# Optimization experiments

Hardware: AMD Instinct MI355X
Metric: run time of the kernel (lower is better)

The kernel has to match this reference:

```python
import jax, jax.numpy as jnp
import numpy as np

SPARSITY = 0.8  # fraction of weights zeroed (random unstructured mask)

def setup_inputs() -> dict:
    key = jax.random.key(0)
    k1, k2, k3, k4 = jax.random.split(key, 4)
    B, S, D_IN, D_OUT = 4, 2048, 4096, 4096
    x = jax.random.normal(k1, (B, S, D_IN), dtype=jnp.float32)
    weight = jax.random.normal(k2, (D_OUT, D_IN), dtype=jnp.float32) * 0.02
    bias = jax.random.normal(k3, (D_OUT,), dtype=jnp.float32) * 0.02
    # fixed binary mask: keep with prob (1 - sparsity)
    mask = (jax.random.uniform(k4, (D_OUT, D_IN)) >= SPARSITY).astype(jnp.float32)
    return {"x": x, "weight": weight, "bias": bias, "mask": mask}

def reference(x, weight, bias, mask):
    # w = weight * mask; y = x @ w.T + b   (F.linear semantics)
    w = weight * mask                      # [O, I]
    y = jnp.einsum('bsi,oi->bso', x, w)    # [B, S, O]
    return y + bias
```

## Files before the change

kernel.cpp:

```cpp
#include <hip/hip_runtime.h>
#include <hip/hip_bf16.h>
#include <stdint.h>

#define M_DIM 8192
#define N_DIM 4096
#define K_DIM 4096
#define BM 128
#define BN 128
#define BK 32

typedef __attribute__((ext_vector_type(8))) __bf16 bf16x8;
typedef __attribute__((ext_vector_type(4))) float floatx4;

__device__ inline unsigned f2b(float f) {
    union { float f; unsigned u; } v; v.f = f;
    return (v.u + 0x7FFFu + ((v.u >> 16) & 1u)) >> 16;
}
__device__ inline unsigned pk2(float lo, float hi) {
    return (f2b(lo) & 0xFFFFu) | (f2b(hi) << 16);
}

__device__ inline void async_load16(const void* g, void* l) {
    __builtin_amdgcn_global_load_lds(
        (const __attribute__((address_space(1))) unsigned int*)(unsigned long long)g,
        (__attribute__((address_space(3))) unsigned int*)(unsigned int)(unsigned long long)l,
        16, 0, 0);
}

__global__ __launch_bounds__(256)
void cvt_x_kernel(const float4* __restrict__ in, uint4* __restrict__ out, int n8) {
    int i = blockIdx.x * blockDim.x + threadIdx.x;
    if (i >= n8) return;
    float4 a = in[2 * i], b = in[2 * i + 1];
    uint4 o;
    o.x = pk2(a.x, a.y); o.y = pk2(a.z, a.w);
    o.z = pk2(b.x, b.y); o.w = pk2(b.z, b.w);
    out[i] = o;
}

__global__ __launch_bounds__(256)
void cvt_w_kernel(const float4* __restrict__ w, const float4* __restrict__ m,
                  uint4* __restrict__ out, int n8) {
    int i = blockIdx.x * blockDim.x + threadIdx.x;
    if (i >= n8) return;
    float4 w0 = w[2 * i], w1 = w[2 * i + 1];
    float4 m0 = m[2 * i], m1 = m[2 * i + 1];
    uint4 o;
    o.x = pk2(w0.x * m0.x, w0.y * m0.y);
    o.y = pk2(w0.z * m0.z, w0.w * m0.w);
    o.z = pk2(w1.x * m1.x, w1.y * m1.y);
    o.w = pk2(w1.z * m1.z, w1.w * m1.w);
    out[i] = o;
}

__global__ __launch_bounds__(256)
void gemm_bt_bias(const __hip_bfloat16* __restrict__ A,
                  const __hip_bfloat16* __restrict__ B,
                  const float* __restrict__ bias,
                  float* __restrict__ C) {
    __shared__ __hip_bfloat16 As[BM * BK];
    __shared__ __hip_bfloat16 Bs[BN * BK];

    const int t    = threadIdx.x;
    const int lane = t & 63;
    const int wave = t >> 6;
    const int wm   = wave >> 1;
    const int wn   = wave & 1;
    const int m0   = blockIdx.y * BM;
    const int n0   = blockIdx.x * BN;

    const int lm = lane & 15;
    const int lk = (lane >> 4) << 3;

    floatx4 acc[4][4] = {};

    const int c0 = t, c1 = t + 256;
    const int ar0 = c0 >> 2, ak0 = (c0 & 3) << 3;
    const int ar1 = c1 >> 2, ak1 = (c1 & 3) << 3;

    const __hip_bfloat16* Ab = A + (size_t)m0 * K_DIM;
    const __hip_bfloat16* Bb = B + (size_t)n0 * K_DIM;

    for (int k0 = 0; k0 < K_DIM; k0 += BK) {
        async_load16(Ab + (size_t)ar0 * K_DIM + k0 + ak0, As + c0 * 8);
        async_load16(Ab + (size_t)ar1 * K_DIM + k0 + ak1, As + c1 * 8);
        async_load16(Bb + (size_t)ar0 * K_DIM + k0 + ak0, Bs + c0 * 8);
        async_load16(Bb + (size_t)ar1 * K_DIM + k0 + ak1, Bs + c1 * 8);
        __syncthreads();

        bf16x8 af[4], bfr[4];
#pragma unroll
        for (int i = 0; i < 4; i++)
            af[i] = *reinterpret_cast<const bf16x8*>(
                &As[(wm * 64 + i * 16 + lm) * BK + lk]);
#pragma unroll
        for (int j = 0; j < 4; j++)
            bfr[j] = *reinterpret_cast<const bf16x8*>(
                &Bs[(wn * 64 + j * 16 + lm) * BK + lk]);
#pragma unroll
        for (int i = 0; i < 4; i++)
#pragma unroll
            for (int j = 0; j < 4; j++)
                acc[i][j] = __builtin_amdgcn_mfma_f32_16x16x32_bf16(
                    af[i], bfr[j], acc[i][j], 0, 0, 0);
        __syncthreads();
    }

    float bv[4];
#pragma unroll
    for (int j = 0; j < 4; j++)
        bv[j] = bias[n0 + wn * 64 + j * 16 + lm];
    const int row_base = m0 + wm * 64 + (lane >> 4) * 4;
    const int col_base = n0 + wn * 64 + lm;
#pragma unroll
    for (int i = 0; i < 4; i++)
#pragma unroll
        for (int j = 0; j < 4; j++) {
            const int col = col_base + j * 16;
#pragma unroll
            for (int r = 0; r < 4; r++)
                C[(size_t)(row_base + i * 16 + r) * N_DIM + col] =
                    acc[i][j][r] + bv[j];
        }
}

__global__ __launch_bounds__(256)
void gemm_fused_f32(const float* __restrict__ A, const float* __restrict__ W,
                    const float* __restrict__ Mk, const float* __restrict__ bias,
                    float* __restrict__ C) {
    __shared__ __hip_bfloat16 As[BM * BK];
    __shared__ __hip_bfloat16 Bs[BN * BK];

    const int t    = threadIdx.x;
    const int lane = t & 63;
    const int wave = t >> 6;
    const int wm   = wave >> 1;
    const int wn   = wave & 1;
    const int m0   = blockIdx.y * BM;
    const int n0   = blockIdx.x * BN;
    const int lm = lane & 15;
    const int lk = (lane >> 4) << 3;

    floatx4 acc[4][4] = {};

    const int r  = t >> 1;
    const int cb = (t & 1) * 16;

    for (int k0 = 0; k0 < K_DIM; k0 += BK) {
        const float* ap = A + (size_t)(m0 + r) * K_DIM + k0 + cb;
        float4 f0 = ((const float4*)ap)[0], f1 = ((const float4*)ap)[1];
        float4 f2 = ((const float4*)ap)[2], f3 = ((const float4*)ap)[3];
        uint4 pa, pb;
        pa.x = pk2(f0.x, f0.y); pa.y = pk2(f0.z, f0.w);
        pa.z = pk2(f1.x, f1.y); pa.w = pk2(f1.z, f1.w);
        pb.x = pk2(f2.x, f2.y); pb.y = pk2(f2.z, f2.w);
        pb.z = pk2(f3.x, f3.y); pb.w = pk2(f3.z, f3.w);
        *(uint4*)&As[r * BK + cb] = pa;
        *(uint4*)&As[r * BK + cb + 8] = pb;

        const float* wp = W + (size_t)(n0 + r) * K_DIM + k0 + cb;
        const float* mp = Mk + (size_t)(n0 + r) * K_DIM + k0 + cb;
        float4 w0 = ((const float4*)wp)[0], w1 = ((const float4*)wp)[1];
        float4 w2 = ((const float4*)wp)[2], w3 = ((const float4*)wp)[3];
        float4 q0 = ((const float4*)mp)[0], q1 = ((const float4*)mp)[1];
        float4 q2 = ((const float4*)mp)[2], q3 = ((const float4*)mp)[3];
        pa.x = pk2(w0.x * q0.x, w0.y * q0.y); pa.y = pk2(w0.z * q0.z, w0.w * q0.w);
        pa.z = pk2(w1.x * q1.x, w1.y * q1.y); pa.w = pk2(w1.z * q1.z, w1.w * q1.w);
        pb.x = pk2(w2.x * q2.x, w2.y * q2.y); pb.y = pk2(w2.z * q2.z, w2.w * q2.w);
        pb.z = pk2(w3.x * q3.x, w3.y * q3.y); pb.w = pk2(w3.z * q3.z, w3.w * q3.w);
        *(uint4*)&Bs[r * BK + cb] = pa;
        *(uint4*)&Bs[r * BK + cb + 8] = pb;
        __syncthreads();

        bf16x8 af[4], bfr[4];
#pragma unroll
        for (int i = 0; i < 4; i++)
            af[i] = *reinterpret_cast<const bf16x8*>(
                &As[(wm * 64 + i * 16 + lm) * BK + lk]);
#pragma unroll
        for (int j = 0; j < 4; j++)
            bfr[j] = *reinterpret_cast<const bf16x8*>(
                &Bs[(wn * 64 + j * 16 + lm) * BK + lk]);
#pragma unroll
        for (int i = 0; i < 4; i++)
#pragma unroll
            for (int j = 0; j < 4; j++)
                acc[i][j] = __builtin_amdgcn_mfma_f32_16x16x32_bf16(
                    af[i], bfr[j], acc[i][j], 0, 0, 0);
        __syncthreads();
    }

    float bv[4];
#pragma unroll
    for (int j = 0; j < 4; j++)
        bv[j] = bias[n0 + wn * 64 + j * 16 + lm];
    const int row_base = m0 + wm * 64 + (lane >> 4) * 4;
    const int col_base = n0 + wn * 64 + lm;
#pragma unroll
    for (int i = 0; i < 4; i++)
#pragma unroll
        for (int j = 0; j < 4; j++) {
            const int col = col_base + j * 16;
#pragma unroll
            for (int r4 = 0; r4 < 4; r4++)
                C[(size_t)(row_base + i * 16 + r4) * N_DIM + col] =
                    acc[i][j][r4] + bv[j];
        }
}

extern "C" void kernel_launch(void* const* d_in, const int* in_sizes, int n_in,
                              void* d_out, int out_size, void* d_ws, size_t ws_size,
                              hipStream_t stream) {
    const float* x    = (const float*)d_in[0];
    const float* w    = (const float*)d_in[1];
    const float* bias = (const float*)d_in[2];
    const float* mask = (const float*)d_in[3];
    float* out = (float*)d_out;

    const size_t xb_bytes = (size_t)M_DIM * K_DIM * 2;
    const size_t wb_bytes = (size_t)N_DIM * K_DIM * 2;
    dim3 grid(N_DIM / BN, M_DIM / BM);
    dim3 block(256);

    if (ws_size >= xb_bytes + wb_bytes) {
        __hip_bfloat16* xb = (__hip_bfloat16*)d_ws;
        __hip_bfloat16* wb = (__hip_bfloat16*)((char*)d_ws + xb_bytes);

        const int nx8 = M_DIM * K_DIM / 8;
        cvt_x_kernel<<<dim3(nx8 / 256), block, 0, stream>>>(
            (const float4*)x, (uint4*)xb, nx8);
        const int nw8 = N_DIM * K_DIM / 8;
        cvt_w_kernel<<<dim3(nw8 / 256), block, 0, stream>>>(
            (const float4*)w, (const float4*)mask, (uint4*)wb, nw8);
        gemm_bt_bias<<<grid, block, 0, stream>>>(xb, wb, bias, out);
    } else {
        gemm_fused_f32<<<grid, block, 0, stream>>>(x, w, mask, bias, out);
    }
}
```

Measured before the change: 624.3 us.

## Pre-pack bf16 operands into swizzled tile panels and merge conversion kernels

```diff
diff --git a/kernel.cpp b/kernel.cpp
--- a/kernel.cpp
+++ b/kernel.cpp
@@ -8,6 +8,8 @@
 #define BM 128
 #define BN 128
 #define BK 32
+#define KP (K_DIM / BK)
+#define PANEL_U4 512
 
 typedef __attribute__((ext_vector_type(8))) __bf16 bf16x8;
 typedef __attribute__((ext_vector_type(4))) float floatx4;
@@ -18,6 +20,12 @@
 }
 __device__ inline unsigned pk2(float lo, float hi) {
     return (f2b(lo) & 0xFFFFu) | (f2b(hi) << 16);
+}
+__device__ inline uint4 pk8(float4 a, float4 b) {
+    uint4 o;
+    o.x = pk2(a.x, a.y); o.y = pk2(a.z, a.w);
+    o.z = pk2(b.x, b.y); o.w = pk2(b.z, b.w);
+    return o;
 }
 
 __device__ inline void async_load16(const void* g, void* l) {
@@ -28,34 +36,42 @@
 }
 
 __global__ __launch_bounds__(256)
-void cvt_x_kernel(const float4* __restrict__ in, uint4* __restrict__ out, int n8) {
-    int i = blockIdx.x * blockDim.x + threadIdx.x;
-    if (i >= n8) return;
-    float4 a = in[2 * i], b = in[2 * i + 1];
-    uint4 o;
-    o.x = pk2(a.x, a.y); o.y = pk2(a.z, a.w);
-    o.z = pk2(b.x, b.y); o.w = pk2(b.z, b.w);
-    out[i] = o;
+void cvt_pack_kernel(const float* __restrict__ x,
+                     const float* __restrict__ w,
+                     const float* __restrict__ mask,
+                     uint4* __restrict__ xb, uint4* __restrict__ wb) {
+    const int NX = M_DIM * K_DIM / 8;
+    int tid = blockIdx.x * 256 + threadIdx.x;
+    if (tid < NX) {
+        const int cx = tid;
+        const int p = cx >> 9, s = cx & 511;
+        const int r4 = s >> 2, perm = s & 3;
+        const int ksub = perm ^ ((r4 >> 1) & 3);
+        const int rt = p >> 7, kp = p & (KP - 1);
+        const size_t src = (size_t)(rt * BM + r4) * K_DIM + kp * BK + ksub * 8;
+        float4 a = *(const float4*)(x + src);
+        float4 b = *(const float4*)(x + src + 4);
+        xb[cx] = pk8(a, b);
+    } else {
+        const int cw = tid - NX;
+        const int p = cw >> 9, s = cw & 511;
+        const int r4 = s >> 2, perm = s & 3;
+        const int ksub = perm ^ ((r4 >> 1) & 3);
+        const int nt = p >> 7, kp = p & (KP - 1);
+        const size_t src = (size_t)(nt * BN + r4) * K_DIM + kp * BK + ksub * 8;
+        float4 a = *(const float4*)(w + src);
+        float4 b = *(const float4*)(w + src + 4);
+        float4 qa = *(const float4*)(mask + src);
+        float4 qb = *(const float4*)(mask + src + 4);
+        a.x *= qa.x; a.y *= qa.y; a.z *= qa.z; a.w *= qa.w;
+        b.x *= qb.x; b.y *= qb.y; b.z *= qb.z; b.w *= qb.w;
+        wb[cw] = pk8(a, b);
+    }
 }
 
 __global__ __launch_bounds__(256)
-void cvt_w_kernel(const float4* __restrict__ w, const float4* __restrict__ m,
-                  uint4* __restrict__ out, int n8) {
-    int i = blockIdx.x * blockDim.x + threadIdx.x;
-    if (i >= n8) return;
-    float4 w0 = w[2 * i], w1 = w[2 * i + 1];
-    float4 m0 = m[2 * i], m1 = m[2 * i + 1];
-    uint4 o;
-    o.x = pk2(w0.x * m0.x, w0.y * m0.y);
-    o.y = pk2(w0.z * m0.z, w0.w * m0.w);
-    o.z = pk2(w1.x * m1.x, w1.y * m1.y);
-    o.w = pk2(w1.z * m1.z, w1.w * m1.w);
-    out[i] = o;
-}
-
-__global__ __launch_bounds__(256)
-void gemm_bt_bias(const __hip_bfloat16* __restrict__ A,
-                  const __hip_bfloat16* __restrict__ B,
+void gemm_bt_bias(const uint4* __restrict__ Apan,
+                  const uint4* __restrict__ Bpan,
                   const float* __restrict__ bias,
                   float* __restrict__ C) {
     __shared__ __hip_bfloat16 As[BM * BK];
@@ -69,34 +85,31 @@
     const int m0   = blockIdx.y * BM;
     const int n0   = blockIdx.x * BN;
 
-    const int lm = lane & 15;
-    const int lk = (lane >> 4) << 3;
+    const int lm   = lane & 15;
+    const int perm = ((lane >> 4) ^ ((lane >> 1) & 3)) & 3;
 
     floatx4 acc[4][4] = {};
 
     const int c0 = t, c1 = t + 256;
-    const int ar0 = c0 >> 2, ak0 = (c0 & 3) << 3;
-    const int ar1 = c1 >> 2, ak1 = (c1 & 3) << 3;
-
-    const __hip_bfloat16* Ab = A + (size_t)m0 * K_DIM;
-    const __hip_bfloat16* Bb = B + (size_t)n0 * K_DIM;
-
-    for (int k0 = 0; k0 < K_DIM; k0 += BK) {
-        async_load16(Ab + (size_t)ar0 * K_DIM + k0 + ak0, As + c0 * 8);
-        async_load16(Ab + (size_t)ar1 * K_DIM + k0 + ak1, As + c1 * 8);
-        async_load16(Bb + (size_t)ar0 * K_DIM + k0 + ak0, Bs + c0 * 8);
-        async_load16(Bb + (size_t)ar1 * K_DIM + k0 + ak1, Bs + c1 * 8);
+    const uint4* ap = Apan + ((size_t)blockIdx.y * KP) * PANEL_U4;
+    const uint4* bp = Bpan + ((size_t)blockIdx.x * KP) * PANEL_U4;
+
+    const __hip_bfloat16* aF = As + (((wm * 64 + lm) * 4 + perm) * 8);
+    const __hip_bfloat16* bF = Bs + (((wn * 64 + lm) * 4 + perm) * 8);
+
+    for (int kp = 0; kp < KP; kp++) {
+        async_load16(ap + c0, As + c0 * 8);
+        async_load16(ap + c1, As + c1 * 8);
+        async_load16(bp + c0, Bs + c0 * 8);
+        async_load16(bp + c1, Bs + c1 * 8);
+        ap += PANEL_U4; bp += PANEL_U4;
         __syncthreads();
 
         bf16x8 af[4], bfr[4];
 #pragma unroll
-        for (int i = 0; i < 4; i++)
-            af[i] = *reinterpret_cast<const bf16x8*>(
-                &As[(wm * 64 + i * 16 + lm) * BK + lk]);
-#pragma unroll
-        for (int j = 0; j < 4; j++)
-            bfr[j] = *reinterpret_cast<const bf16x8*>(
-                &Bs[(wn * 64 + j * 16 + lm) * BK + lk]);
+        for (int i = 0; i < 4; i++) af[i]  = *(const bf16x8*)(aF + i * 512);
+#pragma unroll
+        for (int j = 0; j < 4; j++) bfr[j] = *(const bf16x8*)(bF + j * 512);
 #pragma unroll
         for (int i = 0; i < 4; i++)
 #pragma unroll
@@ -130,57 +143,38 @@
                     float* __restrict__ C) {
     __shared__ __hip_bfloat16 As[BM * BK];
     __shared__ __hip_bfloat16 Bs[BN * BK];
-
-    const int t    = threadIdx.x;
-    const int lane = t & 63;
-    const int wave = t >> 6;
-    const int wm   = wave >> 1;
-    const int wn   = wave & 1;
-    const int m0   = blockIdx.y * BM;
-    const int n0   = blockIdx.x * BN;
-    const int lm = lane & 15;
-    const int lk = (lane >> 4) << 3;
-
+    const int t = threadIdx.x, lane = t & 63, wave = t >> 6;
+    const int wm = wave >> 1, wn = wave & 1;
+    const int m0 = blockIdx.y * BM, n0 = blockIdx.x * BN;
+    const int lm = lane & 15, lk = (lane >> 4) << 3;
     floatx4 acc[4][4] = {};
-
-    const int r  = t >> 1;
-    const int cb = (t & 1) * 16;
-
+    const int r = t >> 1, cb = (t & 1) * 16;
     for (int k0 = 0; k0 < K_DIM; k0 += BK) {
         const float* ap = A + (size_t)(m0 + r) * K_DIM + k0 + cb;
         float4 f0 = ((const float4*)ap)[0], f1 = ((const float4*)ap)[1];
         float4 f2 = ((const float4*)ap)[2], f3 = ((const float4*)ap)[3];
-        uint4 pa, pb;
-        pa.x = pk2(f0.x, f0.y); pa.y = pk2(f0.z, f0.w);
-        pa.z = pk2(f1.x, f1.y); pa.w = pk2(f1.z, f1.w);
-        pb.x = pk2(f2.x, f2.y); pb.y = pk2(f2.z, f2.w);
-        pb.z = pk2(f3.x, f3.y); pb.w = pk2(f3.z, f3.w);
-        *(uint4*)&As[r * BK + cb] = pa;
-        *(uint4*)&As[r * BK + cb + 8] = pb;
-
+        *(uint4*)&As[r * BK + cb] = pk8(f0, f1);
+        *(uint4*)&As[r * BK + cb + 8] = pk8(f2, f3);
         const float* wp = W + (size_t)(n0 + r) * K_DIM + k0 + cb;
         const float* mp = Mk + (size_t)(n0 + r) * K_DIM + k0 + cb;
         float4 w0 = ((const float4*)wp)[0], w1 = ((const float4*)wp)[1];
         float4 w2 = ((const float4*)wp)[2], w3 = ((const float4*)wp)[3];
         float4 q0 = ((const float4*)mp)[0], q1 = ((const float4*)mp)[1];
         float4 q2 = ((const float4*)mp)[2], q3 = ((const float4*)mp)[3];
-        pa.x = pk2(w0.x * q0.x, w0.y * q0.y); pa.y = pk2(w0.z * q0.z, w0.w * q0.w);
-        pa.z = pk2(w1.x * q1.x, w1.y * q1.y); pa.w = pk2(w1.z * q1.z, w1.w * q1.w);
-        pb.x = pk2(w2.x * q2.x, w2.y * q2.y); pb.y = pk2(w2.z * q2.z, w2.w * q2.w);
-        pb.z = pk2(w3.x * q3.x, w3.y * q3.y); pb.w = pk2(w3.z * q3.z, w3.w * q3.w);
-        *(uint4*)&Bs[r * BK + cb] = pa;
-        *(uint4*)&Bs[r * BK + cb + 8] = pb;
-        __syncthreads();
-
+        w0.x*=q0.x; w0.y*=q0.y; w0.z*=q0.z; w0.w*=q0.w;
+        w1.x*=q1.x; w1.y*=q1.y; w1.z*=q1.z; w1.w*=q1.w;
+        w2.x*=q2.x; w2.y*=q2.y; w2.z*=q2.z; w2.w*=q2.w;
+        w3.x*=q3.x; w3.y*=q3.y; w3.z*=q3.z; w3.w*=q3.w;
+        *(uint4*)&Bs[r * BK + cb] = pk8(w0, w1);
+        *(uint4*)&Bs[r * BK + cb + 8] = pk8(w2, w3);
+        __syncthreads();
         bf16x8 af[4], bfr[4];
 #pragma unroll
         for (int i = 0; i < 4; i++)
-            af[i] = *reinterpret_cast<const bf16x8*>(
-                &As[(wm * 64 + i * 16 + lm) * BK + lk]);
+            af[i] = *(const bf16x8*)(&As[(wm * 64 + i * 16 + lm) * BK + lk]);
 #pragma unroll
         for (int j = 0; j < 4; j++)
-            bfr[j] = *reinterpret_cast<const bf16x8*>(
-                &Bs[(wn * 64 + j * 16 + lm) * BK + lk]);
+            bfr[j] = *(const bf16x8*)(&Bs[(wn * 64 + j * 16 + lm) * BK + lk]);
 #pragma unroll
         for (int i = 0; i < 4; i++)
 #pragma unroll
@@ -189,11 +183,9 @@
                     af[i], bfr[j], acc[i][j], 0, 0, 0);
         __syncthreads();
     }
-
     float bv[4];
 #pragma unroll
-    for (int j = 0; j < 4; j++)
-        bv[j] = bias[n0 + wn * 64 + j * 16 + lm];
+    for (int j = 0; j < 4; j++) bv[j] = bias[n0 + wn * 64 + j * 16 + lm];
     const int row_base = m0 + wm * 64 + (lane >> 4) * 4;
     const int col_base = n0 + wn * 64 + lm;
 #pragma unroll
@@ -223,15 +215,11 @@
     dim3 block(256);
 
     if (ws_size >= xb_bytes + wb_bytes) {
-        __hip_bfloat16* xb = (__hip_bfloat16*)d_ws;
-        __hip_bfloat16* wb = (__hip_bfloat16*)((char*)d_ws + xb_bytes);
-
-        const int nx8 = M_DIM * K_DIM / 8;
-        cvt_x_kernel<<<dim3(nx8 / 256), block, 0, stream>>>(
-            (const float4*)x, (uint4*)xb, nx8);
-        const int nw8 = N_DIM * K_DIM / 8;
-        cvt_w_kernel<<<dim3(nw8 / 256), block, 0, stream>>>(
-            (const float4*)w, (const float4*)mask, (uint4*)wb, nw8);
+        uint4* xb = (uint4*)d_ws;
+        uint4* wb = (uint4*)((char*)d_ws + xb_bytes);
+        const int nchunks = (M_DIM * K_DIM + N_DIM * K_DIM) / 8;
+        cvt_pack_kernel<<<dim3(nchunks / 256), block, 0, stream>>>(
+            x, w, mask, xb, wb);
         gemm_bt_bias<<<grid, block, 0, stream>>>(xb, wb, bias, out);
     } else {
         gemm_fused_f32<<<grid, block, 0, stream>>>(x, w, mask, bias, out);
```

Measured after the change: 653.4 us. 4.7% more time.
